# Kernel optimization log

Measured on AMD Instinct MI355X. Metric: run time of the kernel, lower is better.

Reference implementation:

```python
import jax, jax.numpy as jnp
import numpy as np

P = 4       # patch size
NQ = 6      # qubits (2**6 = 64 amplitudes)
NH = 8      # classic attention heads
HD = 8      # head dim (64 / 8)
EPS = 1e-9

_SIGNS = (1.0 - 2.0 * (((np.arange(64)[:, None] >> np.arange(NQ - 1, -1, -1)[None, :]) & 1))).astype(np.float32)  # [64, 6] Z-expectation signs, wire 0 = MSB


def _ln(x, g, b, eps=1e-5):
    m = x.mean(-1, keepdims=True)
    v = x.var(-1, keepdims=True)
    return (x - m) / jnp.sqrt(v + eps) * g + b


def _rot_rx(t):
    c = jnp.cos(t / 2).astype(jnp.complex64)
    s = jnp.sin(t / 2).astype(jnp.complex64)
    return jnp.stack([jnp.stack([c, -1j * s]), jnp.stack([-1j * s, c])])


def _rot_ry(t):
    c = jnp.cos(t / 2).astype(jnp.complex64)
    s = jnp.sin(t / 2).astype(jnp.complex64)
    return jnp.stack([jnp.stack([c, -s]), jnp.stack([s, c])])


def _apply_1q(psi, g, wire):
    # psi: [bsz, 2,2,2,2,2,2]; apply 2x2 unitary g on one wire
    ax = wire + 1
    psi = jnp.moveaxis(psi, ax, -1)
    psi = jnp.einsum('ab,...b->...a', g, psi)
    return jnp.moveaxis(psi, -1, ax)


def _cnot(psi, i):
    # CNOT on adjacent wires [i, i+1]
    cax = i + 1
    p0 = jnp.take(psi, 0, axis=cax)
    p1 = jnp.take(psi, 1, axis=cax)
    p1 = jnp.flip(p1, axis=cax)  # target axis i+2 shifts to cax after removing control axis
    return jnp.stack([p0, p1], axis=cax)


def _pqc(psi, w):
    # RX+RY -> CNOT chain -> RY per layer; w: [depth, NQ, 3]
    for l in range(w.shape[0]):
        for q in range(NQ):
            psi = _apply_1q(psi, _rot_rx(w[l, q, 0]), q)
            psi = _apply_1q(psi, _rot_ry(w[l, q, 1]), q)
        for q in range(NQ - 1):
            psi = _cnot(psi, q)
        for q in range(NQ):
            psi = _apply_1q(psi, _rot_ry(w[l, q, 2]), q)
    return psi


def _probs(psi):
    f = psi.reshape(psi.shape[0], 64)
    return f.real ** 2 + f.imag ** 2


def _measure_z(psi):
    return _probs(psi) @ jnp.asarray(_SIGNS)  # [bsz, 6]


def setup_inputs() -> dict:
    key = jax.random.key(0)
    k = lambda i: jax.random.fold_in(key, i)
    n = lambda i, shp, s=0.02: jax.random.normal(k(i), shp, jnp.float32) * s
    return dict(
        x=jax.random.normal(k(0), (16, 4, 128, 128), jnp.float32),
        conv_w=n(1, (384, 4, P, P)), conv_b=jnp.zeros((384,), jnp.float32),
        ln1_g=jnp.ones(64), ln1_b=jnp.zeros(64),
        wq=n(2, (64, 64)), wk=n(3, (64, 64)), wv=n(4, (64, 64)), wo=n(5, (64, 64)), bo=jnp.zeros(64),
        ln2_g=jnp.ones(64), ln2_b=jnp.zeros(64),
        enc_w=n(6, (2, NQ, 3), 0.1), q_w=n(7, (2, NQ, 3), 0.1), k_w=n(8, (2, NQ, 3), 0.1), v_w=n(9, (2, NQ, 3), 0.1),
        meas_q_w=n(10, (NQ, 3), 0.1), meas_k_w=n(11, (NQ, 3), 0.1), meas_v_w=n(12, (NQ, 3), 0.1),
        qproj_w=n(13, (4, NQ), 0.1), qproj_b=jnp.zeros(4),
        kproj_w=n(14, (4, NQ), 0.1), kproj_b=jnp.zeros(4),
        qkln_g=jnp.ones(4), qkln_b=jnp.zeros(4),
        raw_tau=jnp.asarray(np.log(np.exp(0.5) - 1.0), jnp.float32),
        inp_scale=jnp.ones(64),
        ln3_g=jnp.ones(64), ln3_b=jnp.zeros(64),
        mlp_w1=n(15, (256, 64)), mlp_b1=jnp.zeros(256), mlp_w2=n(16, (64, 256)), mlp_b2=jnp.zeros(64),
    )


def reference(x, conv_w, conv_b, ln1_g, ln1_b, wq, wk, wv, wo, bo, ln2_g, ln2_b,
              enc_w, q_w, k_w, v_w, meas_q_w, meas_k_w, meas_v_w,
              qproj_w, qproj_b, kproj_w, kproj_b, qkln_g, qkln_b, raw_tau, inp_scale,
              ln3_g, ln3_b, mlp_w1, mlp_b1, mlp_w2, mlp_b2):
    B, C, H, W = x.shape
    Hp, Wp = H // P, W // P
    L = Hp * Wp

    # --- PatchEmbed2D: DiT-style conv tokens [B, L, 384] ---
    t384 = jax.lax.conv_general_dilated(x, conv_w, (P, P), 'VALID',
                                        dimension_numbers=('NCHW', 'OIHW', 'NCHW'))
    t384 = t384.reshape(B, -1, L).transpose(0, 2, 1) + conv_b

    # --- PatchEmbed2D: unfold -> amplitude-normalized 64-d tokens ---
    t64 = x.reshape(B, C, Hp, P, Wp, P).transpose(0, 2, 4, 1, 3, 5).reshape(B, L, C * P * P)
    t64 = t64 / (jnp.linalg.norm(t64, axis=-1, keepdims=True) + EPS)

    # --- ClassicAttention64 (manual einsum + softmax MHSA) ---
    hin = _ln(t64, ln1_g, ln1_b)
    q = (hin @ wq.T).reshape(B, L, NH, HD).transpose(0, 2, 1, 3)
    kk = (hin @ wk.T).reshape(B, L, NH, HD).transpose(0, 2, 1, 3)
    v = (hin @ wv.T).reshape(B, L, NH, HD).transpose(0, 2, 1, 3)
    logits = jnp.einsum('bhid,bhjd->bhij', q, kk) * (HD ** -0.5)
    attn = jax.nn.softmax(logits, axis=-1)
    out = jnp.einsum('bhij,bhjd->bhid', attn, v).transpose(0, 2, 1, 3).reshape(B, L, 64)
    h = t64 + (out @ wo.T + bo)

    # --- QuantumAttention64 (QSANN, RBF kernel attention) ---
    xq = _ln(h, ln2_g, ln2_b) * inp_scale
    st = xq.reshape(B * L, 64)
    st = st / (jnp.linalg.norm(st, axis=-1, keepdims=True) + EPS)
    psi0 = st.astype(jnp.complex64).reshape((B * L,) + (2,) * NQ)
    psi_enc = _pqc(psi0, enc_w)
    zq = _measure_z(_pqc(_pqc(psi_enc, q_w), meas_q_w[None]))
    zk = _measure_z(_pqc(_pqc(psi_enc, k_w), meas_k_w[None]))
    pv = _probs(_pqc(_pqc(psi_enc, v_w), meas_v_w[None]))
    v64 = (pv / (pv.sum(-1, keepdims=True) + EPS)).reshape(B, L, 64)
    qv = _ln(zq @ qproj_w.T + qproj_b, qkln_g, qkln_b).reshape(B, L, -1)
    kv = _ln(zk @ kproj_w.T + kproj_b, qkln_g, qkln_b).reshape(B, L, -1)
    tau = jax.nn.softplus(raw_tau)
    d2 = jnp.maximum((qv ** 2).sum(-1)[:, :, None] + (kv ** 2).sum(-1)[:, None, :]
                     - 2.0 * jnp.einsum('bid,bjd->bij', qv, kv), 0.0)
    alpha = jnp.exp(-d2 / tau)
    wts = alpha / (alpha.sum(-1, keepdims=True) + EPS)
    h = h + jnp.einsum('bij,bjd->bid', wts, v64)

    # --- MLP (64 -> 256 -> 64, GELU) ---
    hm = _ln(h, ln3_g, ln3_b)
    h = h + (jax.nn.gelu(hm @ mlp_w1.T + mlp_b1, approximate=True) @ mlp_w2.T + mlp_b2)

    # combine both streams into a single output tensor [B, L, 448]
    return jnp.concatenate([t384, h], axis=-1)
```

## Files before the change

kernel.cpp:

```cpp
#include <hip/hip_runtime.h>

typedef float4 f4;
#define DEV static __device__ __forceinline__

constexpr int Ln = 1024;
constexpr float EPSn = 1e-9f;

typedef __attribute__((ext_vector_type(8))) short short8;
typedef __attribute__((ext_vector_type(16))) float f32x16;
typedef __attribute__((ext_vector_type(4))) unsigned int u32x4;

constexpr size_t OFF_T64 = 0;
constexpr size_t OFF_H   = 1048576;
constexpr size_t OFF_Q   = 2097152;
constexpr size_t OFF_K   = 3145728;
constexpr size_t OFF_V   = 4194304;
constexpr size_t OFF_AO  = 5242880;
constexpr size_t OFF_TR  = 6291456;
constexpr size_t OFF_WQT = OFF_TR + 24576;
constexpr size_t OFF_WKT = OFF_WQT + 4096;
constexpr size_t OFF_WVT = OFF_WKT + 4096;
constexpr size_t OFF_WOT = OFF_WVT + 4096;
constexpr size_t OFF_U   = OFF_WOT + 4096;
constexpr size_t OFF_W2P = OFF_U + 1024;
constexpr size_t OFF_W1P = OFF_W2P + 16384;
constexpr size_t OFF_UT  = OFF_W1P + 16384;

DEV float red16(float v) {
  v += __shfl_xor(v, 1); v += __shfl_xor(v, 2);
  v += __shfl_xor(v, 4); v += __shfl_xor(v, 8);
  return v;
}

DEV unsigned int pk_bf16(float lo, float hi) {
  unsigned int r;
  asm("v_cvt_pk_bf16_f32 %0, %1, %2" : "=v"(r) : "v"(lo), "v"(hi));
  return r;
}

DEV float fast_exp2(float x) {
#if __has_builtin(__builtin_amdgcn_exp2f)
  return __builtin_amdgcn_exp2f(x);
#else
  return __expf(x * 0.6931471805599453f);
#endif
}

__global__ __launch_bounds__(256) void prep_transpose_kernel(
    const float* __restrict__ conv_w, const float* __restrict__ wq,
    const float* __restrict__ wk, const float* __restrict__ wv,
    const float* __restrict__ wo, const float* __restrict__ w1,
    const float* __restrict__ w2, float* __restrict__ ws) {
  int g = blockIdx.x * 256 + threadIdx.x;
  if (g < 24576) {
    int kk = g / 384, o = g % 384;
    ws[OFF_TR + g] = conv_w[o * 64 + kk];
  } else if (g < 40960) {
    int i = g - 24576;
    int m = i >> 12;
    int r = i & 4095;
    int d = r >> 6, o = r & 63;
    const float* src = m == 0 ? wq : m == 1 ? wk : m == 2 ? wv : wo;
    ws[OFF_WQT + i] = src[o * 64 + d];
  } else if (g < 57344) {
    int i = g - 40960;
    int u4 = i >> 8, r = i & 255, o = r >> 2, j = r & 3;
    ws[OFF_W2P + i] = w2[o * 256 + u4 * 4 + j];
  } else if (g < 73728) {
    int i = g - 57344;
    int d4 = i >> 10, r = i & 1023, u = r >> 2, j = r & 3;
    ws[OFF_W1P + i] = w1[u * 64 + d4 * 4 + j];
  }
}

DEV void cmulc(float ar, float ai, float br, float bi, float& cr, float& ci) {
  cr = ar * br - ai * bi; ci = ar * bi + ai * br;
}
DEV void mat2mul(const float* A, const float* B, float* C) {
  for (int i = 0; i < 2; ++i)
    for (int j = 0; j < 2; ++j) {
      float sr = 0.f, si = 0.f;
      for (int kk = 0; kk < 2; ++kk) {
        float pr, pi;
        cmulc(A[(i * 2 + kk) * 2], A[(i * 2 + kk) * 2 + 1],
              B[(kk * 2 + j) * 2], B[(kk * 2 + j) * 2 + 1], pr, pi);
        sr += pr; si += pi;
      }
      C[(i * 2 + j) * 2] = sr; C[(i * 2 + j) * 2 + 1] = si;
    }
}
__global__ void prep_u_kernel(const float* __restrict__ enc_w, const float* __restrict__ q_w,
                              const float* __restrict__ k_w, const float* __restrict__ v_w,
                              const float* __restrict__ mq, const float* __restrict__ mk,
                              const float* __restrict__ mv, float* __restrict__ U) {
  int j = threadIdx.x;
  if (j >= 108) return;
  int branch = j / 36, rem = j % 36, blk = rem / 6, wire = rem % 6;
  const float* bw = branch == 0 ? q_w : branch == 1 ? k_w : v_w;
  const float* mw = branch == 0 ? mq : branch == 1 ? mk : mv;
  auto W = [&](int l, int t) -> float {
    if (l <= 1) return enc_w[(l * 6 + wire) * 3 + t];
    if (l <= 3) return bw[((l - 2) * 6 + wire) * 3 + t];
    return mw[wire * 3 + t];
  };
  auto mk_rx = [](float th, float* M) {
    float c = cosf(0.5f * th), s = sinf(0.5f * th);
    M[0] = c; M[1] = 0; M[2] = 0; M[3] = -s; M[4] = 0; M[5] = -s; M[6] = c; M[7] = 0;
  };
  auto mk_ry = [](float th, float* M) {
    float c = cosf(0.5f * th), s = sinf(0.5f * th);
    M[0] = c; M[1] = 0; M[2] = -s; M[3] = 0; M[4] = s; M[5] = 0; M[6] = c; M[7] = 0;
  };
  float R[8];
  if (blk == 0) {
    float A[8], Bx[8];
    mk_ry(W(0, 1), A); mk_rx(W(0, 0), Bx);
    mat2mul(A, Bx, R);
  } else if (blk <= 4) {
    float A[8], Bx[8], C[8], T[8];
    mk_ry(W(blk, 1), A); mk_rx(W(blk, 0), Bx); mk_ry(W(blk - 1, 2), C);
    mat2mul(Bx, C, T); mat2mul(A, T, R);
  } else {
    mk_ry(W(4, 2), R);
  }
  float* dst = U + ((size_t)(branch * 6 + blk) * 6 + wire) * 8;
  for (int t = 0; t < 8; ++t) dst[t] = R[t];
}

__global__ __launch_bounds__(64) void prep_ubuild_kernel(const float* __restrict__ U,
                                                         float* __restrict__ ut) {
  int branch = blockIdx.x;
  int quad = blockIdx.y;
  int tid = threadIdx.x;
  int s = tid & 3;
  int lane = tid;
  int c = quad * 16 + (tid >> 2);
  bool bit1 = (s & 2) != 0;
  bool bit0 = (s & 1) != 0;
  float re[16], im[16];
#pragma unroll
  for (int i = 0; i < 16; ++i) { re[i] = (s * 16 + i == c) ? 1.f : 0.f; im[i] = 0.f; }
  const float* Ub = U + (size_t)branch * 288;
#pragma unroll 1
  for (int blk = 0; blk < 6; ++blk) {
    const float* Uw = Ub + blk * 48;
    {
      const float* M = Uw;
      float cAr = bit1 ? M[6] : M[0], cAi = bit1 ? M[7] : M[1];
      float cBr = bit1 ? M[4] : M[2], cBi = bit1 ? M[5] : M[3];
#pragma unroll
      for (int i = 0; i < 16; ++i) {
        float pr = __shfl_xor(re[i], 2);
        float pi = __shfl_xor(im[i], 2);
        float nr = cAr * re[i] - cAi * im[i] + cBr * pr - cBi * pi;
        float ni = cAr * im[i] + cAi * re[i] + cBr * pi + cBi * pr;
        re[i] = nr; im[i] = ni;
      }
    }
    {
      const float* M = Uw + 8;
      float cAr = bit0 ? M[6] : M[0], cAi = bit0 ? M[7] : M[1];
      float cBr = bit0 ? M[4] : M[2], cBi = bit0 ? M[5] : M[3];
#pragma unroll
      for (int i = 0; i < 16; ++i) {
        float pr = __shfl_xor(re[i], 1);
        float pi = __shfl_xor(im[i], 1);
        float nr = cAr * re[i] - cAi * im[i] + cBr * pr - cBi * pi;
        float ni = cAr * im[i] + cAi * re[i] + cBr * pi + cBi * pr;
        re[i] = nr; im[i] = ni;
      }
    }
#pragma unroll
    for (int w = 2; w < 6; ++w) {
      const float* M = Uw + w * 8;
      const float m0 = M[0], m1 = M[1], m2 = M[2], m3 = M[3];
      const float m4 = M[4], m5 = M[5], m6 = M[6], m7 = M[7];
      const int mm = 8 >> (w - 2);
#pragma unroll
      for (int i = 0; i < 16; ++i) {
        if (i & mm) continue;
        int i1 = i | mm;
        float ar = re[i], ai = im[i], br = re[i1], bi = im[i1];
        re[i]  = m0 * ar - m1 * ai + m2 * br - m3 * bi;
        im[i]  = m0 * ai + m1 * ar + m2 * bi + m3 * br;
        re[i1] = m4 * ar - m5 * ai + m6 * br - m7 * bi;
        im[i1] = m4 * ai + m5 * ar + m6 * bi + m7 * br;
      }
    }
    if (blk < 5) {
      int sl = (lane & ~3) | (bit1 ? (s ^ 1) : s);
      float tr[16], ti[16];
#pragma unroll
      for (int i = 0; i < 16; ++i) {
        tr[i] = __shfl(re[i], sl);
        ti[i] = __shfl(im[i], sl);
      }
#pragma unroll
      for (int i = 0; i < 16; ++i) {
        int j = i;
        if (j & 2) j ^= 1;
        if (j & 4) j ^= 2;
        if (j & 8) j ^= 4;
        re[i] = bit0 ? tr[j ^ 8] : tr[j];
        im[i] = bit0 ? ti[j ^ 8] : ti[j];
      }
    }
  }
  float* dre = ut + (size_t)branch * 8192 + c * 64 + s * 16;
  float* dim = dre + 4096;
#pragma unroll
  for (int i = 0; i < 16; i += 4) {
    f4 r4 = {re[i], re[i + 1], re[i + 2], re[i + 3]};
    f4 i4 = {im[i], im[i + 1], im[i + 2], im[i + 3]};
    *(f4*)(dre + i) = r4;
    *(f4*)(dim + i) = i4;
  }
}

__global__ __launch_bounds__(256) void patch_kernel(const float* __restrict__ x,
    const float* __restrict__ cwT, const float* __restrict__ conv_b,
    float* __restrict__ out, float* __restrict__ t64) {
  __shared__ float A[64][72];
  __shared__ float scl[64];
  int tid = threadIdx.x;
  int tb = blockIdx.x >> 1;
  int half = blockIdx.x & 1;
  int b = tb >> 4;
  int l0 = (tb & 15) << 6;
  int seg = tid & 15;
  int c = seg >> 2, ph = seg & 3;
#pragma unroll
  for (int r = 0; r < 4; ++r) {
    int tok = (tid >> 4) + (r << 4);
    int l = l0 + tok, hp = l >> 5, wp = l & 31;
    f4 v4 = *(const f4*)(x + (size_t)((b * 4 + c) * 128 + hp * 4 + ph) * 128 + wp * 4);
    A[seg * 4 + 0][tok] = v4.x;
    A[seg * 4 + 1][tok] = v4.y;
    A[seg * 4 + 2][tok] = v4.z;
    A[seg * 4 + 3][tok] = v4.w;
  }
  __syncthreads();
  if (tid < 64) {
    float ss = 0.f;
#pragma unroll
    for (int kk = 0; kk < 64; ++kk) { float vv = A[kk][tid]; ss += vv * vv; }
    scl[tid] = 1.0f / (sqrtf(ss) + EPSn);
  }
  __syncthreads();
  int t0 = tb << 6;
  if (half == 0) {
#pragma unroll
    for (int i = 0; i < 16; ++i) {
      int idx = tid + (i << 8);
      int tok = idx >> 6, kk = idx & 63;
      t64[(size_t)(t0 + tok) * 64 + kk] = A[kk][tok] * scl[tok];
    }
  }
  int tg = tid >> 4;
  int on = (tid & 15) + half * 16;
  float acc[4][12];
#pragma unroll
  for (int i = 0; i < 4; ++i)
#pragma unroll
    for (int jj = 0; jj < 12; ++jj) acc[i][jj] = 0.f;
  for (int kk = 0; kk < 64; ++kk) {
    float a[4];
#pragma unroll
    for (int i = 0; i < 4; ++i) a[i] = A[kk][tg * 4 + i];
    f4 w0 = *(const f4*)(cwT + kk * 384 + on * 12);
    f4 w1 = *(const f4*)(cwT + kk * 384 + on * 12 + 4);
    f4 w2 = *(const f4*)(cwT + kk * 384 + on * 12 + 8);
    float wv_[12] = {w0.x, w0.y, w0.z, w0.w, w1.x, w1.y, w1.z, w1.w, w2.x, w2.y, w2.z, w2.w};
#pragma unroll
    for (int i = 0; i < 4; ++i)
#pragma unroll
      for (int jj = 0; jj < 12; ++jj) acc[i][jj] += a[i] * wv_[jj];
  }
#pragma unroll
  for (int i = 0; i < 4; ++i) {
    int tok = tg * 4 + i;
    size_t basep = (size_t)(t0 + tok) * 448 + on * 12;
#pragma unroll
    for (int jj = 0; jj < 12; ++jj)
      out[basep + jj] = acc[i][jj] + conv_b[on * 12 + jj];
  }
}

__global__ __launch_bounds__(256) void qkv_kernel(const float* __restrict__ t64,
    const float* __restrict__ wqT, const float* __restrict__ wkT, const float* __restrict__ wvT,
    const float* __restrict__ g1, const float* __restrict__ b1,
    float* __restrict__ qo, float* __restrict__ ko, float* __restrict__ vo) {
  __shared__ float wS[12288];
  __shared__ float hin[16][64];
  int tid = threadIdx.x;
#pragma unroll
  for (int p = 0; p < 16; ++p) {
    int idx = p * 256 + tid;
    wS[idx] = wqT[idx];
    wS[4096 + idx] = wkT[idx];
    wS[8192 + idx] = wvT[idx];
  }
  int t0 = blockIdx.x << 4;
  int tt = tid >> 4, part = tid & 15;
  int t = t0 + tt;
  f4 xv = *(const f4*)(t64 + (size_t)t * 64 + part * 4);
  float mean = red16(xv.x + xv.y + xv.z + xv.w) * 0.015625f;
  float d0 = xv.x - mean, d1 = xv.y - mean, d2 = xv.z - mean, d3 = xv.w - mean;
  float var = red16(d0 * d0 + d1 * d1 + d2 * d2 + d3 * d3) * 0.015625f;
  float rs = rsqrtf(var + 1e-5f);
  f4 g4 = *(const f4*)(g1 + part * 4);
  f4 b4 = *(const f4*)(b1 + part * 4);
  f4 hh;
  hh.x = d0 * rs * g4.x + b4.x; hh.y = d1 * rs * g4.y + b4.y;
  hh.z = d2 * rs * g4.z + b4.z; hh.w = d3 * rs * g4.w + b4.w;
  *(f4*)&hin[tt][part * 4] = hh;
  __syncthreads();
  float qa0 = 0, qa1 = 0, qa2 = 0, qa3 = 0;
  float ka0 = 0, ka1 = 0, ka2 = 0, ka3 = 0;
  float va0 = 0, va1 = 0, va2 = 0, va3 = 0;
  for (int d = 0; d < 64; ++d) {
    float hd = hin[tt][d];
    f4 wq4 = *(const f4*)&wS[d * 64 + part * 4];
    f4 wk4 = *(const f4*)&wS[4096 + d * 64 + part * 4];
    f4 wv4 = *(const f4*)&wS[8192 + d * 64 + part * 4];
    qa0 += hd * wq4.x; qa1 += hd * wq4.y; qa2 += hd * wq4.z; qa3 += hd * wq4.w;
    ka0 += hd * wk4.x; ka1 += hd * wk4.y; ka2 += hd * wk4.z; ka3 += hd * wk4.w;
    va0 += hd * wv4.x; va1 += hd * wv4.y; va2 += hd * wv4.z; va3 += hd * wv4.w;
  }
  f4 qr = {qa0, qa1, qa2, qa3}, kr = {ka0, ka1, ka2, ka3}, vr = {va0, va1, va2, va3};
  *(f4*)(qo + (size_t)t * 64 + part * 4) = qr;
  *(f4*)(ko + (size_t)t * 64 + part * 4) = kr;
  *(f4*)(vo + (size_t)t * 64 + part * 4) = vr;
}

__global__ __launch_bounds__(256) void attn_kernel(const float* __restrict__ qg,
    const float* __restrict__ kg, const float* __restrict__ vg, float* __restrict__ ao) {
  __shared__ __align__(16) unsigned short Klds[Ln][8];
  __shared__ __align__(16) unsigned short Vt[10][1032];
  __shared__ __align__(16) unsigned short Qlds[128][8];
  int bh = blockIdx.x;
  int b = bh >> 3, hh = bh & 7;
  int tid = threadIdx.x;
  int qbase = (blockIdx.y << 7);
  const float* kb = kg + (size_t)(b * Ln) * 64 + hh * 8;
  const float* vb = vg + (size_t)(b * Ln) * 64 + hh * 8;
  const float* qb = qg + (size_t)(b * Ln + qbase) * 64 + hh * 8;
  const float SC = 0.51006944f;
#pragma unroll
  for (int p = 0; p < 8; ++p) {
    int e4 = p * 256 + tid;
    int j = e4 >> 1, part = e4 & 1;
    f4 kv = *(const f4*)(kb + (size_t)j * 64 + part * 4);
    *(uint2*)&Klds[j][part * 4] =
        make_uint2(pk_bf16(kv.x * SC, kv.y * SC), pk_bf16(kv.z * SC, kv.w * SC));
    f4 vv = *(const f4*)(vb + (size_t)j * 64 + part * 4);
    unsigned int u01 = pk_bf16(vv.x, vv.y), u23 = pk_bf16(vv.z, vv.w);
    int d0 = part * 4;
    Vt[d0 + 0][j] = (unsigned short)u01;
    Vt[d0 + 1][j] = (unsigned short)(u01 >> 16);
    Vt[d0 + 2][j] = (unsigned short)u23;
    Vt[d0 + 3][j] = (unsigned short)(u23 >> 16);
  }
#pragma unroll
  for (int p = 0; p < 4; ++p) {
    int j = p * 256 + tid;
    Vt[8][j] = 0x3F80;
    Vt[9][j] = 0;
  }
  {
    int j = tid >> 1, part = tid & 1;
    f4 qv = *(const f4*)(qb + (size_t)j * 64 + part * 4);
    *(uint2*)&Qlds[j][part * 4] = make_uint2(pk_bf16(qv.x, qv.y), pk_bf16(qv.z, qv.w));
  }
  __syncthreads();

  int l = tid & 63, w = tid >> 6;
  int lq = l & 31;
  bool lo = l < 32;
  const short8 zero8 = {0, 0, 0, 0, 0, 0, 0, 0};
  short8 qf = *(const short8*)&Qlds[w * 32 + lq][0];
  qf = lo ? qf : zero8;
  int d = lq;
  int dc = d > 9 ? 9 : d;
  int vrow0 = (l >> 5) * 8;
  f32x16 acc = {};
  const f32x16 fz = {};
  for (int t = 0; t < 32; ++t) {
    short8 kf = *(const short8*)&Klds[t * 32 + lq][0];
    kf = lo ? kf : zero8;
    f32x16 s = __builtin_amdgcn_mfma_f32_32x32x16_bf16(kf, qf, fz, 0, 0, 0);
    float p[16];
#pragma unroll
    for (int r = 0; r < 16; ++r) p[r] = fast_exp2(s[r]);
    unsigned int c0 = pk_bf16(p[0], p[1]),  c1 = pk_bf16(p[2], p[3]);
    unsigned int c2 = pk_bf16(p[4], p[5]),  c3 = pk_bf16(p[6], p[7]);
    unsigned int c4 = pk_bf16(p[8], p[9]),  c5 = pk_bf16(p[10], p[11]);
    unsigned int c6 = pk_bf16(p[12], p[13]), c7 = pk_bf16(p[14], p[15]);
    unsigned int x0 = c0, y0 = c2;
    asm("v_permlane32_swap_b32 %0, %1" : "+v"(x0), "+v"(y0));
    unsigned int x1 = c1, y1 = c3;
    asm("v_permlane32_swap_b32 %0, %1" : "+v"(x1), "+v"(y1));
    unsigned int x4 = c4, y4 = c6;
    asm("v_permlane32_swap_b32 %0, %1" : "+v"(x4), "+v"(y4));
    unsigned int x5 = c5, y5 = c7;
    asm("v_permlane32_swap_b32 %0, %1" : "+v"(x5), "+v"(y5));
    union { u32x4 u; short8 s8; } B0, B1;
    B0.u = (u32x4){x0, x1, y0, y1};
    B1.u = (u32x4){x4, x5, y4, y5};
    int jb = t * 32 + vrow0;
    short8 av0 = *(const short8*)&Vt[dc][jb];
    short8 av1 = *(const short8*)&Vt[dc][jb + 16];
    acc = __builtin_amdgcn_mfma_f32_32x32x16_bf16(av0, B0.s8, acc, 0, 0, 0);
    acc = __builtin_amdgcn_mfma_f32_32x32x16_bf16(av1, B1.s8, acc, 0, 0, 0);
  }
  float ssum = __shfl(acc[4], lq);
  float inv = 1.0f / ssum;
  f4 o = {acc[0] * inv, acc[1] * inv, acc[2] * inv, acc[3] * inv};
  float* dst = ao + (size_t)(b * Ln + qbase + w * 32 + lq) * 64 + hh * 8 + (lo ? 0 : 4);
  *(f4*)dst = o;
}

__global__ __launch_bounds__(256) void proj_st_kernel(float* __restrict__ t64st,
    const float* __restrict__ ao, const float* __restrict__ woT, const float* __restrict__ bo,
    const float* __restrict__ g2, const float* __restrict__ b2, const float* __restrict__ iscale,
    float* __restrict__ hB) {
  __shared__ float woS[4096];
  __shared__ float aos[16][64];
  int tid = threadIdx.x;
#pragma unroll
  for (int p = 0; p < 16; ++p) {
    int idx = p * 256 + tid;
    woS[idx] = woT[idx];
  }
  int t0 = blockIdx.x << 4;
  int tt = tid >> 4, part = tid & 15;
  int t = t0 + tt;
  *(f4*)&aos[tt][part * 4] = *(const f4*)(ao + (size_t)t * 64 + part * 4);
  __syncthreads();
  f4 acc;
  acc.x = bo[part * 4 + 0]; acc.y = bo[part * 4 + 1];
  acc.z = bo[part * 4 + 2]; acc.w = bo[part * 4 + 3];
  for (int d = 0; d < 64; ++d) {
    float ad = aos[tt][d];
    f4 w4 = *(const f4*)&woS[d * 64 + part * 4];
    acc.x += ad * w4.x; acc.y += ad * w4.y; acc.z += ad * w4.z; acc.w += ad * w4.w;
  }
  f4 tv = *(const f4*)(t64st + (size_t)t * 64 + part * 4);
  f4 hv = {tv.x + acc.x, tv.y + acc.y, tv.z + acc.z, tv.w + acc.w};
  *(f4*)(hB + (size_t)t * 64 + part * 4) = hv;
  float mean = red16(hv.x + hv.y + hv.z + hv.w) * 0.015625f;
  float d0 = hv.x - mean, d1 = hv.y - mean, d2 = hv.z - mean, d3 = hv.w - mean;
  float var = red16(d0 * d0 + d1 * d1 + d2 * d2 + d3 * d3) * 0.015625f;
  float rs = rsqrtf(var + 1e-5f);
  f4 g4 = *(const f4*)(g2 + part * 4);
  f4 b4 = *(const f4*)(b2 + part * 4);
  f4 is4 = *(const f4*)(iscale + part * 4);
  float x0 = (d0 * rs * g4.x + b4.x) * is4.x;
  float x1 = (d1 * rs * g4.y + b4.y) * is4.y;
  float x2 = (d2 * rs * g4.z + b4.z) * is4.z;
  float x3 = (d3 * rs * g4.w + b4.w) * is4.w;
  float nrm = sqrtf(red16(x0 * x0 + x1 * x1 + x2 * x2 + x3 * x3));
  float rn = 1.0f / (nrm + EPSn);
  f4 stv = {x0 * rn, x1 * rn, x2 * rn, x3 * rn};
  *(f4*)(t64st + (size_t)t * 64 + part * 4) = stv;
}

__global__ __launch_bounds__(256) void quantum_kernel(const float* __restrict__ st,
    const float* __restrict__ ut,
    const float* __restrict__ qproj_w, const float* __restrict__ qproj_b,
    const float* __restrict__ kproj_w, const float* __restrict__ kproj_b,
    const float* __restrict__ qkg, const float* __restrict__ qkb,
    float* __restrict__ qvb, float* __restrict__ kvb, float* __restrict__ v64) {
  __shared__ float smem[12288];
  int tid = threadIdx.x;
  int branch = blockIdx.y;
  int t0 = blockIdx.x << 6;
  const float* ub = ut + (size_t)branch * 8192;
#pragma unroll
  for (int p = 0; p < 16; ++p) {
    int idx = p * 256 + tid;
    smem[idx] = st[(size_t)t0 * 64 + idx];
    smem[4096 + idx] = ub[idx];
    smem[8192 + idx] = ub[4096 + idx];
  }
  __syncthreads();
  int o = tid & 63, tg = tid >> 6;
  float accre[16], accim[16];
#pragma unroll
  for (int i = 0; i < 16; ++i) { accre[i] = 0.f; accim[i] = 0.f; }
  for (int k4 = 0; k4 < 16; ++k4) {
    float ur[4], ui[4];
#pragma unroll
    for (int j = 0; j < 4; ++j) {
      ur[j] = smem[4096 + (k4 * 4 + j) * 64 + o];
      ui[j] = smem[8192 + (k4 * 4 + j) * 64 + o];
    }
#pragma unroll
    for (int tt = 0; tt < 16; ++tt) {
      f4 a = *(const f4*)&smem[(tg * 16 + tt) * 64 + k4 * 4];
      accre[tt] += a.x * ur[0] + a.y * ur[1] + a.z * ur[2] + a.w * ur[3];
      accim[tt] += a.x * ui[0] + a.y * ui[1] + a.z * ui[2] + a.w * ui[3];
    }
  }
  __syncthreads();
#pragma unroll
  for (int tt = 0; tt < 16; ++tt) {
    int t = tg * 16 + tt;
    smem[t * 65 + o] = accre[tt] * accre[tt] + accim[tt] * accim[tt];
  }
  __syncthreads();
  int s = tid & 3;
  int tokL = tid >> 2;
  int token = t0 + tokL;
  bool bit1 = (s & 2) != 0;
  bool bit0 = (s & 1) != 0;
  float p[16];
#pragma unroll
  for (int i = 0; i < 16; ++i) p[i] = smem[tokL * 65 + s * 16 + i];
  float lsum = 0.f;
#pragma unroll
  for (int i = 0; i < 16; ++i) lsum += p[i];
  if (branch == 2) {
    float tot = lsum;
    tot += __shfl_xor(tot, 1);
    tot += __shfl_xor(tot, 2);
    float rn = 1.0f / (tot + EPSn);
    float* dst = v64 + (size_t)token * 64 + s * 16;
#pragma unroll
    for (int i = 0; i < 16; i += 4) {
      f4 o4 = {p[i] * rn, p[i + 1] * rn, p[i + 2] * rn, p[i + 3] * rn};
      *(f4*)(dst + i) = o4;
    }
  } else {
    float lz[4] = {0.f, 0.f, 0.f, 0.f};
#pragma unroll
    for (int i = 0; i < 16; ++i) {
      lz[0] += (i & 8) ? -p[i] : p[i];
      lz[1] += (i & 4) ? -p[i] : p[i];
      lz[2] += (i & 2) ? -p[i] : p[i];
      lz[3] += (i & 1) ? -p[i] : p[i];
    }
    float z[6];
    float u0 = bit1 ? -lsum : lsum;
    u0 += __shfl_xor(u0, 1); u0 += __shfl_xor(u0, 2); z[0] = u0;
    float u1 = bit0 ? -lsum : lsum;
    u1 += __shfl_xor(u1, 1); u1 += __shfl_xor(u1, 2); z[1] = u1;
#pragma unroll
    for (int q = 0; q < 4; ++q) {
      float v = lz[q];
      v += __shfl_xor(v, 1); v += __shfl_xor(v, 2);
      z[2 + q] = v;
    }
    const float* pw = branch == 0 ? qproj_w : kproj_w;
    const float* pb = branch == 0 ? qproj_b : kproj_b;
    float pr4[4];
#pragma unroll
    for (int jj = 0; jj < 4; ++jj) {
      float a = pb[jj];
#pragma unroll
      for (int qq = 0; qq < 6; ++qq) a += z[qq] * pw[jj * 6 + qq];
      pr4[jj] = a;
    }
    float mean = (pr4[0] + pr4[1] + pr4[2] + pr4[3]) * 0.25f;
    float var = 0.f;
#pragma unroll
    for (int jj = 0; jj < 4; ++jj) { float dd = pr4[jj] - mean; var += dd * dd; }
    var *= 0.25f;
    float rs = rsqrtf(var + 1e-5f);
    if (s == 0) {
      f4 o4;
      o4.x = (pr4[0] - mean) * rs * qkg[0] + qkb[0];
      o4.y = (pr4[1] - mean) * rs * qkg[1] + qkb[1];
      o4.z = (pr4[2] - mean) * rs * qkg[2] + qkb[2];
      o4.w = (pr4[3] - mean) * rs * qkg[3] + qkb[3];
      *(f4*)((branch == 0 ? qvb : kvb) + (size_t)token * 4) = o4;
    }
  }
}

__global__ __launch_bounds__(256) void rbf_kernel(const float* __restrict__ qvb,
    const float* __restrict__ kvb, const float* __restrict__ v64,
    const float* __restrict__ raw_tau, float* __restrict__ pacc, float* __restrict__ pasum) {
  __shared__ __align__(16) unsigned short Vlds[512][64];
  __shared__ __align__(16) unsigned short kvbs[512][8];
  __shared__ float kks[512];
  int tid = threadIdx.x;
  int q0 = blockIdx.x << 7;
  int b = q0 >> 10;
  int kc = blockIdx.y;
  float tau = log1pf(__expf(raw_tau[0]));
  float inv_tau = 1.0f / tau;
  float inv2t = 2.0f * inv_tau;
  int kbase = b * Ln + (kc << 9);
#pragma unroll
  for (int p = 0; p < 2; ++p) {
    int j = p * 256 + tid;
    f4 kv4 = *(const f4*)(kvb + (size_t)(kbase + j) * 4);
    kks[j] = (kv4.x * kv4.x + kv4.y * kv4.y + kv4.z * kv4.z + kv4.w * kv4.w) * inv_tau;
    *(uint4*)&kvbs[j][0] = make_uint4(pk_bf16(kv4.x, kv4.y), pk_bf16(kv4.z, kv4.w), 0u, 0u);
  }
#pragma unroll
  for (int it = 0; it < 32; ++it) {
    int idx = it * 256 + tid;
    int row = idx >> 4, c4 = idx & 15;
    f4 vv = *(const f4*)(v64 + (size_t)(kbase + row) * 64 + c4 * 4);
    *(uint2*)&Vlds[row][c4 * 4] = make_uint2(pk_bf16(vv.x, vv.y), pk_bf16(vv.z, vv.w));
  }
  __syncthreads();

  int l = tid & 63, w = tid >> 6;
  int lq = l & 31;
  bool lo = l < 32;
  bool hi = !lo;
  const short8 zero8 = {0, 0, 0, 0, 0, 0, 0, 0};
  int qtok = q0 + w * 32 + lq;
  f4 qv4 = *(const f4*)(qvb + (size_t)qtok * 4);
  union { u32x4 u; short8 s8; } Qf;
  Qf.u = (u32x4){pk_bf16(qv4.x, qv4.y), pk_bf16(qv4.z, qv4.w), 0u, 0u};
  short8 qf = lo ? Qf.s8 : zero8;
  int vrow0 = (l >> 5) * 8;
  int dbase = hi ? 4 : 0;
  f32x16 acc0 = {}, acc1 = {};
  const f32x16 fz = {};
  float dsum = 0.f;
  for (int t = 0; t < 16; ++t) {
    short8 kf = lo ? *(const short8*)&kvbs[t * 32 + lq][0] : zero8;
    f32x16 s = __builtin_amdgcn_mfma_f32_32x32x16_bf16(kf, qf, fz, 0, 0, 0);
    int rowbase = t * 32 + dbase;
    float p[16];
#pragma unroll
    for (int r = 0; r < 16; ++r) {
      float kkv = kks[rowbase + (r & 3) + 8 * (r >> 2)];
      p[r] = __expf(s[r] * inv2t - kkv);
      dsum += p[r];
    }
    unsigned int c0 = pk_bf16(p[0], p[1]),  c1 = pk_bf16(p[2], p[3]);
    unsigned int c2 = pk_bf16(p[4], p[5]),  c3 = pk_bf16(p[6], p[7]);
    unsigned int c4 = pk_bf16(p[8], p[9]),  c5 = pk_bf16(p[10], p[11]);
    unsigned int c6 = pk_bf16(p[12], p[13]), c7 = pk_bf16(p[14], p[15]);
    unsigned int pc0 = (unsigned int)__shfl((int)c0, l ^ 32);
    unsigned int pc1 = (unsigned int)__shfl((int)c1, l ^ 32);
    unsigned int pc2 = (unsigned int)__shfl((int)c2, l ^ 32);
    unsigned int pc3 = (unsigned int)__shfl((int)c3, l ^ 32);
    unsigned int pc4 = (unsigned int)__shfl((int)c4, l ^ 32);
    unsigned int pc5 = (unsigned int)__shfl((int)c5, l ^ 32);
    unsigned int pc6 = (unsigned int)__shfl((int)c6, l ^ 32);
    unsigned int pc7 = (unsigned int)__shfl((int)c7, l ^ 32);
    union { u32x4 u; short8 s8; } B0, B1;
    B0.u = lo ? (u32x4){c0, c1, pc0, pc1} : (u32x4){pc2, pc3, c2, c3};
    B1.u = lo ? (u32x4){c4, c5, pc4, pc5} : (u32x4){pc6, pc7, c6, c7};
    int jb = t * 32 + vrow0;
    short8 a00, a10, a01, a11;
#pragma unroll
    for (int e = 0; e < 8; ++e) {
      a00[e] = (short)Vlds[jb + e][lq];
      a10[e] = (short)Vlds[jb + e][32 + lq];
      a01[e] = (short)Vlds[jb + 16 + e][lq];
      a11[e] = (short)Vlds[jb + 16 + e][32 + lq];
    }
    acc0 = __builtin_amdgcn_mfma_f32_32x32x16_bf16(a00, B0.s8, acc0, 0, 0, 0);
    acc1 = __builtin_amdgcn_mfma_f32_32x32x16_bf16(a10, B0.s8, acc1, 0, 0, 0);
    acc0 = __builtin_amdgcn_mfma_f32_32x32x16_bf16(a01, B1.s8, acc0, 0, 0, 0);
    acc1 = __builtin_amdgcn_mfma_f32_32x32x16_bf16(a11, B1.s8, acc1, 0, 0, 0);
  }
  float dtot = dsum + __shfl_xor(dsum, 32);
  if (lo) pasum[(kc << 14) + qtok] = dtot;
  float* pa = pacc + (size_t)kc * 1048576 + (size_t)qtok * 64;
#pragma unroll
  for (int r = 0; r < 16; ++r) {
    int dd = (r & 3) + 8 * (r >> 2) + dbase;
    pa[dd] = acc0[r];
    pa[32 + dd] = acc1[r];
  }
}

__global__ __launch_bounds__(256) void m0m1_kernel(float* __restrict__ hB,
    const float* __restrict__ pacc, const float* __restrict__ pasum,
    const float* __restrict__ g3, const float* __restrict__ b3,
    const float* __restrict__ w1p, const float* __restrict__ b1v,
    float* __restrict__ hid) {
  __shared__ float hmS[16][64];
  int tid = threadIdx.x;
  int t0 = blockIdx.x << 4;
  {
    int tt = tid >> 4, part = tid & 15;
    int t = t0 + tt;
    f4 hv = *(const f4*)(hB + (size_t)t * 64 + part * 4);
    f4 p0 = *(const f4*)(pacc + (size_t)t * 64 + part * 4);
    f4 p1 = *(const f4*)(pacc + 1048576 + (size_t)t * 64 + part * 4);
    float rden = 1.0f / (pasum[t] + pasum[16384 + t] + EPSn);
    hv.x += (p0.x + p1.x) * rden; hv.y += (p0.y + p1.y) * rden;
    hv.z += (p0.z + p1.z) * rden; hv.w += (p0.w + p1.w) * rden;
    *(f4*)(hB + (size_t)t * 64 + part * 4) = hv;
    float mean = red16(hv.x + hv.y + hv.z + hv.w) * 0.015625f;
    float d0 = hv.x - mean, d1 = hv.y - mean, d2 = hv.z - mean, d3 = hv.w - mean;
    float var = red16(d0 * d0 + d1 * d1 + d2 * d2 + d3 * d3) * 0.015625f;
    float rs = rsqrtf(var + 1e-5f);
    f4 g4 = *(const f4*)(g3 + part * 4);
    f4 b4 = *(const f4*)(b3 + part * 4);
    f4 o4 = {d0 * rs * g4.x + b4.x, d1 * rs * g4.y + b4.y,
             d2 * rs * g4.z + b4.z, d3 * rs * g4.w + b4.w};
    *(f4*)&hmS[tt][part * 4] = o4;
  }
  __syncthreads();
  int u = tid;
  float wrow[64];
#pragma unroll
  for (int d4 = 0; d4 < 16; ++d4) {
    f4 w4 = *(const f4*)(w1p + d4 * 1024 + u * 4);
    wrow[d4 * 4] = w4.x; wrow[d4 * 4 + 1] = w4.y;
    wrow[d4 * 4 + 2] = w4.z; wrow[d4 * 4 + 3] = w4.w;
  }
  float bias = b1v[u];
  for (int tok = 0; tok < 16; ++tok) {
    const float* hr = hmS[tok];
    float a0 = 0.f, a1 = 0.f, a2 = 0.f, a3 = 0.f;
#pragma unroll
    for (int d = 0; d < 64; d += 4) {
      a0 += hr[d] * wrow[d];
      a1 += hr[d + 1] * wrow[d + 1];
      a2 += hr[d + 2] * wrow[d + 2];
      a3 += hr[d + 3] * wrow[d + 3];
    }
    float a = bias + ((a0 + a1) + (a2 + a3));
    float tz = 0.7978845608028654f * (a + 0.044715f * a * a * a);
    float e = __expf(2.0f * tz);
    float th = 1.0f - 2.0f / (e + 1.0f);
    hid[(size_t)(t0 + tok) * 256 + u] = 0.5f * a * (1.0f + th);
  }
}

__global__ __launch_bounds__(256) void m2_kernel(const float* __restrict__ hB,
    const float* __restrict__ hid, const float* __restrict__ w2p, const float* __restrict__ b2v,
    float* __restrict__ out) {
  __shared__ float hidS[32][256];
  int tid = threadIdx.x;
  int t0 = blockIdx.x << 5;
#pragma unroll
  for (int p = 0; p < 8; ++p) {
    int idx = p * 256 + tid;
    int tok = idx >> 6, u4 = idx & 63;
    *(f4*)&hidS[tok][u4 * 4] = *(const f4*)(hid + (size_t)(t0 + tok) * 256 + u4 * 4);
  }
  __syncthreads();
  int o = tid & 63, tg = tid >> 6;
  f4 acc[8];
#pragma unroll
  for (int tt = 0; tt < 8; ++tt) acc[tt] = {0.f, 0.f, 0.f, 0.f};
#pragma unroll 4
  for (int u4 = 0; u4 < 64; ++u4) {
    f4 wv = *(const f4*)(w2p + u4 * 256 + o * 4);
#pragma unroll
    for (int tt = 0; tt < 8; ++tt) {
      f4 hv = *(const f4*)&hidS[tg * 8 + tt][u4 * 4];
      acc[tt].x += hv.x * wv.x; acc[tt].y += hv.y * wv.y;
      acc[tt].z += hv.z * wv.z; acc[tt].w += hv.w * wv.w;
    }
  }
  float bb = b2v[o];
#pragma unroll
  for (int tt = 0; tt < 8; ++tt) {
    int t = t0 + tg * 8 + tt;
    float r = bb + ((acc[tt].x + acc[tt].y) + (acc[tt].z + acc[tt].w));
    out[(size_t)t * 448 + 384 + o] = hB[(size_t)t * 64 + o] + r;
  }
}

extern "C" void kernel_launch(void* const* d_in, const int* in_sizes, int n_in,
                              void* d_out, int out_size, void* d_ws, size_t ws_size,
                              hipStream_t stream) {
  (void)in_sizes; (void)n_in; (void)out_size; (void)ws_size;
  const float* x       = (const float*)d_in[0];
  const float* conv_w  = (const float*)d_in[1];
  const float* conv_b  = (const float*)d_in[2];
  const float* ln1_g   = (const float*)d_in[3];
  const float* ln1_b   = (const float*)d_in[4];
  const float* wq      = (const float*)d_in[5];
  const float* wk      = (const float*)d_in[6];
  const float* wv      = (const float*)d_in[7];
  const float* wo      = (const float*)d_in[8];
  const float* bo      = (const float*)d_in[9];
  const float* ln2_g   = (const float*)d_in[10];
  const float* ln2_b   = (const float*)d_in[11];
  const float* enc_w   = (const float*)d_in[12];
  const float* q_w     = (const float*)d_in[13];
  const float* k_w     = (const float*)d_in[14];
  const float* v_w     = (const float*)d_in[15];
  const float* mq_w    = (const float*)d_in[16];
  const float* mk_w    = (const float*)d_in[17];
  const float* mv_w    = (const float*)d_in[18];
  const float* qproj_w = (const float*)d_in[19];
  const float* qproj_b = (const float*)d_in[20];
  const float* kproj_w = (const float*)d_in[21];
  const float* kproj_b = (const float*)d_in[22];
  const float* qkln_g  = (const float*)d_in[23];
  const float* qkln_b  = (const float*)d_in[24];
  const float* raw_tau = (const float*)d_in[25];
  const float* iscale  = (const float*)d_in[26];
  const float* ln3_g   = (const float*)d_in[27];
  const float* ln3_b   = (const float*)d_in[28];
  const float* mlp_w1  = (const float*)d_in[29];
  const float* mlp_b1  = (const float*)d_in[30];
  const float* mlp_w2  = (const float*)d_in[31];
  const float* mlp_b2  = (const float*)d_in[32];
  float* out = (float*)d_out;
  float* ws  = (float*)d_ws;

  prep_transpose_kernel<<<288, 256, 0, stream>>>(conv_w, wq, wk, wv, wo, mlp_w1, mlp_w2, ws);
  prep_u_kernel<<<1, 128, 0, stream>>>(enc_w, q_w, k_w, v_w, mq_w, mk_w, mv_w, ws + OFF_U);
  prep_ubuild_kernel<<<dim3(3, 4), 64, 0, stream>>>(ws + OFF_U, ws + OFF_UT);
  patch_kernel<<<512, 256, 0, stream>>>(x, ws + OFF_TR, conv_b, out, ws + OFF_T64);
  qkv_kernel<<<1024, 256, 0, stream>>>(ws + OFF_T64, ws + OFF_WQT, ws + OFF_WKT, ws + OFF_WVT,
                                       ln1_g, ln1_b, ws + OFF_Q, ws + OFF_K, ws + OFF_V);
  attn_kernel<<<dim3(128, 8), 256, 0, stream>>>(ws + OFF_Q, ws + OFF_K, ws + OFF_V, ws + OFF_AO);
  proj_st_kernel<<<1024, 256, 0, stream>>>(ws + OFF_T64, ws + OFF_AO, ws + OFF_WOT, bo,
                                           ln2_g, ln2_b, iscale, ws + OFF_H);
  quantum_kernel<<<dim3(256, 3), 256, 0, stream>>>(ws + OFF_T64, ws + OFF_UT,
                                                   qproj_w, qproj_b, kproj_w, kproj_b,
                                                   qkln_g, qkln_b,
                                                   ws + OFF_K, ws + OFF_K + 65536, ws + OFF_Q);
  rbf_kernel<<<dim3(128, 2), 256, 0, stream>>>(ws + OFF_K, ws + OFF_K + 65536, ws + OFF_Q,
                                               raw_tau, ws + OFF_V, ws + OFF_K + 131072);
  m0m1_kernel<<<1024, 256, 0, stream>>>(ws + OFF_H, ws + OFF_V, ws + OFF_K + 131072,
                                        ln3_g, ln3_b, ws + OFF_W1P, mlp_b1, ws + OFF_Q);
  m2_kernel<<<512, 256, 0, stream>>>(ws + OFF_H, ws + OFF_Q, ws + OFF_W2P, mlp_b2, out);
}
```

Before: 195.7 us.

## Merge prep kernels into one launch and streamline RBF attention inner loop

Three small weight-preparation launches become one kernel: the gate matrices are built in shared memory and consumed in the same block, which removes two launches and a global round trip. In the RBF kernel, V is stored transposed in LDS so MFMA operands load as single 16-byte vectors instead of eight scalar reads. The 2/tau and log2(e) scaling is folded into the bf16 K operand so the exponential becomes a bare exp2. The eight cross-half shuffles are replaced with four v_permlane32_swap instructions. The transposed LDS fill uses scattered 2-byte stores that may bank-conflict, and folding the scale before bf16 rounding slightly changes numerics.

```diff
diff --git a/kernel.cpp b/kernel.cpp
--- a/kernel.cpp
+++ b/kernel.cpp
@@ -46,33 +46,6 @@
 #endif
 }
 
-__global__ __launch_bounds__(256) void prep_transpose_kernel(
-    const float* __restrict__ conv_w, const float* __restrict__ wq,
-    const float* __restrict__ wk, const float* __restrict__ wv,
-    const float* __restrict__ wo, const float* __restrict__ w1,
-    const float* __restrict__ w2, float* __restrict__ ws) {
-  int g = blockIdx.x * 256 + threadIdx.x;
-  if (g < 24576) {
-    int kk = g / 384, o = g % 384;
-    ws[OFF_TR + g] = conv_w[o * 64 + kk];
-  } else if (g < 40960) {
-    int i = g - 24576;
-    int m = i >> 12;
-    int r = i & 4095;
-    int d = r >> 6, o = r & 63;
-    const float* src = m == 0 ? wq : m == 1 ? wk : m == 2 ? wv : wo;
-    ws[OFF_WQT + i] = src[o * 64 + d];
-  } else if (g < 57344) {
-    int i = g - 40960;
-    int u4 = i >> 8, r = i & 255, o = r >> 2, j = r & 3;
-    ws[OFF_W2P + i] = w2[o * 256 + u4 * 4 + j];
-  } else if (g < 73728) {
-    int i = g - 57344;
-    int d4 = i >> 10, r = i & 1023, u = r >> 2, j = r & 3;
-    ws[OFF_W1P + i] = w1[u * 64 + d4 * 4 + j];
-  }
-}
-
 DEV void cmulc(float ar, float ai, float br, float bi, float& cr, float& ci) {
   cr = ar * br - ai * bi; ci = ar * bi + ai * br;
 }
@@ -89,49 +62,78 @@
       C[(i * 2 + j) * 2] = sr; C[(i * 2 + j) * 2 + 1] = si;
     }
 }
-__global__ void prep_u_kernel(const float* __restrict__ enc_w, const float* __restrict__ q_w,
-                              const float* __restrict__ k_w, const float* __restrict__ v_w,
-                              const float* __restrict__ mq, const float* __restrict__ mk,
-                              const float* __restrict__ mv, float* __restrict__ U) {
-  int j = threadIdx.x;
-  if (j >= 108) return;
-  int branch = j / 36, rem = j % 36, blk = rem / 6, wire = rem % 6;
+
+__global__ __launch_bounds__(256) void prep_all_kernel(
+    const float* __restrict__ conv_w, const float* __restrict__ wq,
+    const float* __restrict__ wk, const float* __restrict__ wv,
+    const float* __restrict__ wo, const float* __restrict__ w1,
+    const float* __restrict__ w2,
+    const float* __restrict__ enc_w, const float* __restrict__ q_w,
+    const float* __restrict__ k_w, const float* __restrict__ v_w,
+    const float* __restrict__ mq, const float* __restrict__ mk,
+    const float* __restrict__ mv, float* __restrict__ ws) {
+  __shared__ float Ulds[288];
+  int bx = blockIdx.x;
+  int tid = threadIdx.x;
+  if (bx < 288) {
+    int g = bx * 256 + tid;
+    if (g < 24576) {
+      int kk = g / 384, o = g % 384;
+      ws[OFF_TR + g] = conv_w[o * 64 + kk];
+    } else if (g < 40960) {
+      int i = g - 24576;
+      int m = i >> 12;
+      int r = i & 4095;
+      int d = r >> 6, o = r & 63;
+      const float* src = m == 0 ? wq : m == 1 ? wk : m == 2 ? wv : wo;
+      ws[OFF_WQT + i] = src[o * 64 + d];
+    } else if (g < 57344) {
+      int i = g - 40960;
+      int u4 = i >> 8, r = i & 255, o = r >> 2, j = r & 3;
+      ws[OFF_W2P + i] = w2[o * 256 + u4 * 4 + j];
+    } else if (g < 73728) {
+      int i = g - 57344;
+      int d4 = i >> 10, r = i & 1023, u = r >> 2, j = r & 3;
+      ws[OFF_W1P + i] = w1[u * 64 + d4 * 4 + j];
+    }
+    return;
+  }
+  int ub = bx - 288;
+  int branch = ub >> 2, quad = ub & 3;
   const float* bw = branch == 0 ? q_w : branch == 1 ? k_w : v_w;
   const float* mw = branch == 0 ? mq : branch == 1 ? mk : mv;
-  auto W = [&](int l, int t) -> float {
-    if (l <= 1) return enc_w[(l * 6 + wire) * 3 + t];
-    if (l <= 3) return bw[((l - 2) * 6 + wire) * 3 + t];
-    return mw[wire * 3 + t];
-  };
-  auto mk_rx = [](float th, float* M) {
-    float c = cosf(0.5f * th), s = sinf(0.5f * th);
-    M[0] = c; M[1] = 0; M[2] = 0; M[3] = -s; M[4] = 0; M[5] = -s; M[6] = c; M[7] = 0;
-  };
-  auto mk_ry = [](float th, float* M) {
-    float c = cosf(0.5f * th), s = sinf(0.5f * th);
-    M[0] = c; M[1] = 0; M[2] = -s; M[3] = 0; M[4] = s; M[5] = 0; M[6] = c; M[7] = 0;
-  };
-  float R[8];
-  if (blk == 0) {
-    float A[8], Bx[8];
-    mk_ry(W(0, 1), A); mk_rx(W(0, 0), Bx);
-    mat2mul(A, Bx, R);
-  } else if (blk <= 4) {
-    float A[8], Bx[8], C[8], T[8];
-    mk_ry(W(blk, 1), A); mk_rx(W(blk, 0), Bx); mk_ry(W(blk - 1, 2), C);
-    mat2mul(Bx, C, T); mat2mul(A, T, R);
-  } else {
-    mk_ry(W(4, 2), R);
-  }
-  float* dst = U + ((size_t)(branch * 6 + blk) * 6 + wire) * 8;
-  for (int t = 0; t < 8; ++t) dst[t] = R[t];
-}
-
-__global__ __launch_bounds__(64) void prep_ubuild_kernel(const float* __restrict__ U,
-                                                         float* __restrict__ ut) {
-  int branch = blockIdx.x;
-  int quad = blockIdx.y;
-  int tid = threadIdx.x;
+  if (tid < 36) {
+    int blk = tid / 6, wire = tid % 6;
+    auto W = [&](int l, int t) -> float {
+      if (l <= 1) return enc_w[(l * 6 + wire) * 3 + t];
+      if (l <= 3) return bw[((l - 2) * 6 + wire) * 3 + t];
+      return mw[wire * 3 + t];
+    };
+    auto mk_rx = [](float th, float* M) {
+      float c = cosf(0.5f * th), s = sinf(0.5f * th);
+      M[0] = c; M[1] = 0; M[2] = 0; M[3] = -s; M[4] = 0; M[5] = -s; M[6] = c; M[7] = 0;
+    };
+    auto mk_ry = [](float th, float* M) {
+      float c = cosf(0.5f * th), s = sinf(0.5f * th);
+      M[0] = c; M[1] = 0; M[2] = -s; M[3] = 0; M[4] = s; M[5] = 0; M[6] = c; M[7] = 0;
+    };
+    float R[8];
+    if (blk == 0) {
+      float A[8], Bx[8];
+      mk_ry(W(0, 1), A); mk_rx(W(0, 0), Bx);
+      mat2mul(A, Bx, R);
+    } else if (blk <= 4) {
+      float A[8], Bx[8], C[8], T[8];
+      mk_ry(W(blk, 1), A); mk_rx(W(blk, 0), Bx); mk_ry(W(blk - 1, 2), C);
+      mat2mul(Bx, C, T); mat2mul(A, T, R);
+    } else {
+      mk_ry(W(4, 2), R);
+    }
+#pragma unroll
+    for (int t = 0; t < 8; ++t) Ulds[(blk * 6 + wire) * 8 + t] = R[t];
+  }
+  __syncthreads();
+  if (tid >= 64) return;
   int s = tid & 3;
   int lane = tid;
   int c = quad * 16 + (tid >> 2);
@@ -140,10 +142,9 @@
   float re[16], im[16];
 #pragma unroll
   for (int i = 0; i < 16; ++i) { re[i] = (s * 16 + i == c) ? 1.f : 0.f; im[i] = 0.f; }
-  const float* Ub = U + (size_t)branch * 288;
 #pragma unroll 1
   for (int blk = 0; blk < 6; ++blk) {
-    const float* Uw = Ub + blk * 48;
+    const float* Uw = Ulds + blk * 48;
     {
       const float* M = Uw;
       float cAr = bit1 ? M[6] : M[0], cAi = bit1 ? M[7] : M[1];
@@ -206,7 +207,7 @@
       }
     }
   }
-  float* dre = ut + (size_t)branch * 8192 + c * 64 + s * 16;
+  float* dre = ws + OFF_UT + (size_t)branch * 8192 + c * 64 + s * 16;
   float* dim = dre + 4096;
 #pragma unroll
   for (int i = 0; i < 16; i += 4) {
@@ -581,7 +582,7 @@
 __global__ __launch_bounds__(256) void rbf_kernel(const float* __restrict__ qvb,
     const float* __restrict__ kvb, const float* __restrict__ v64,
     const float* __restrict__ raw_tau, float* __restrict__ pacc, float* __restrict__ pasum) {
-  __shared__ __align__(16) unsigned short Vlds[512][64];
+  __shared__ __align__(16) unsigned short Vt[64][520];
   __shared__ __align__(16) unsigned short kvbs[512][8];
   __shared__ float kks[512];
   int tid = threadIdx.x;
@@ -589,22 +590,28 @@
   int b = q0 >> 10;
   int kc = blockIdx.y;
   float tau = log1pf(__expf(raw_tau[0]));
-  float inv_tau = 1.0f / tau;
-  float inv2t = 2.0f * inv_tau;
+  const float L2E = 1.4426950408889634f;
+  float sck = 2.0f * L2E / tau;
   int kbase = b * Ln + (kc << 9);
 #pragma unroll
   for (int p = 0; p < 2; ++p) {
     int j = p * 256 + tid;
     f4 kv4 = *(const f4*)(kvb + (size_t)(kbase + j) * 4);
-    kks[j] = (kv4.x * kv4.x + kv4.y * kv4.y + kv4.z * kv4.z + kv4.w * kv4.w) * inv_tau;
-    *(uint4*)&kvbs[j][0] = make_uint4(pk_bf16(kv4.x, kv4.y), pk_bf16(kv4.z, kv4.w), 0u, 0u);
+    kks[j] = (kv4.x * kv4.x + kv4.y * kv4.y + kv4.z * kv4.z + kv4.w * kv4.w) * (L2E / tau);
+    *(uint4*)&kvbs[j][0] =
+        make_uint4(pk_bf16(kv4.x * sck, kv4.y * sck), pk_bf16(kv4.z * sck, kv4.w * sck), 0u, 0u);
   }
 #pragma unroll
   for (int it = 0; it < 32; ++it) {
     int idx = it * 256 + tid;
     int row = idx >> 4, c4 = idx & 15;
     f4 vv = *(const f4*)(v64 + (size_t)(kbase + row) * 64 + c4 * 4);
-    *(uint2*)&Vlds[row][c4 * 4] = make_uint2(pk_bf16(vv.x, vv.y), pk_bf16(vv.z, vv.w));
+    unsigned int u01 = pk_bf16(vv.x, vv.y), u23 = pk_bf16(vv.z, vv.w);
+    int d0 = c4 * 4;
+    Vt[d0 + 0][row] = (unsigned short)u01;
+    Vt[d0 + 1][row] = (unsigned short)(u01 >> 16);
+    Vt[d0 + 2][row] = (unsigned short)u23;
+    Vt[d0 + 3][row] = (unsigned short)(u23 >> 16);
   }
   __syncthreads();
 
@@ -631,33 +638,29 @@
 #pragma unroll
     for (int r = 0; r < 16; ++r) {
       float kkv = kks[rowbase + (r & 3) + 8 * (r >> 2)];
-      p[r] = __expf(s[r] * inv2t - kkv);
+      p[r] = fast_exp2(s[r] - kkv);
       dsum += p[r];
     }
     unsigned int c0 = pk_bf16(p[0], p[1]),  c1 = pk_bf16(p[2], p[3]);
     unsigned int c2 = pk_bf16(p[4], p[5]),  c3 = pk_bf16(p[6], p[7]);
     unsigned int c4 = pk_bf16(p[8], p[9]),  c5 = pk_bf16(p[10], p[11]);
     unsigned int c6 = pk_bf16(p[12], p[13]), c7 = pk_bf16(p[14], p[15]);
-    unsigned int pc0 = (unsigned int)__shfl((int)c0, l ^ 32);
-    unsigned int pc1 = (unsigned int)__shfl((int)c1, l ^ 32);
-    unsigned int pc2 = (unsigned int)__shfl((int)c2, l ^ 32);
-    unsigned int pc3 = (unsigned int)__shfl((int)c3, l ^ 32);
-    unsigned int pc4 = (unsigned int)__shfl((int)c4, l ^ 32);
-    unsigned int pc5 = (unsigned int)__shfl((int)c5, l ^ 32);
-    unsigned int pc6 = (unsigned int)__shfl((int)c6, l ^ 32);
-    unsigned int pc7 = (unsigned int)__shfl((int)c7, l ^ 32);
+    unsigned int x0 = c0, y0 = c2;
+    asm("v_permlane32_swap_b32 %0, %1" : "+v"(x0), "+v"(y0));
+    unsigned int x1 = c1, y1 = c3;
+    asm("v_permlane32_swap_b32 %0, %1" : "+v"(x1), "+v"(y1));
+    unsigned int x4 = c4, y4 = c6;
+    asm("v_permlane32_swap_b32 %0, %1" : "+v"(x4), "+v"(y4));
+    unsigned int x5 = c5, y5 = c7;
+    asm("v_permlane32_swap_b32 %0, %1" : "+v"(x5), "+v"(y5));
     union { u32x4 u; short8 s8; } B0, B1;
-    B0.u = lo ? (u32x4){c0, c1, pc0, pc1} : (u32x4){pc2, pc3, c2, c3};
-    B1.u = lo ? (u32x4){c4, c5, pc4, pc5} : (u32x4){pc6, pc7, c6, c7};
+    B0.u = (u32x4){x0, x1, y0, y1};
+    B1.u = (u32x4){x4, x5, y4, y5};
     int jb = t * 32 + vrow0;
-    short8 a00, a10, a01, a11;
-#pragma unroll
-    for (int e = 0; e < 8; ++e) {
-      a00[e] = (short)Vlds[jb + e][lq];
-      a10[e] = (short)Vlds[jb + e][32 + lq];
-      a01[e] = (short)Vlds[jb + 16 + e][lq];
-      a11[e] = (short)Vlds[jb + 16 + e][32 + lq];
-    }
+    short8 a00 = *(const short8*)&Vt[lq][jb];
+    short8 a10 = *(const short8*)&Vt[32 + lq][jb];
+    short8 a01 = *(const short8*)&Vt[lq][jb + 16];
+    short8 a11 = *(const short8*)&Vt[32 + lq][jb + 16];
     acc0 = __builtin_amdgcn_mfma_f32_32x32x16_bf16(a00, B0.s8, acc0, 0, 0, 0);
     acc1 = __builtin_amdgcn_mfma_f32_32x32x16_bf16(a10, B0.s8, acc1, 0, 0, 0);
     acc0 = __builtin_amdgcn_mfma_f32_32x32x16_bf16(a01, B1.s8, acc0, 0, 0, 0);
@@ -806,9 +809,8 @@
   float* out = (float*)d_out;
   float* ws  = (float*)d_ws;
 
-  prep_transpose_kernel<<<288, 256, 0, stream>>>(conv_w, wq, wk, wv, wo, mlp_w1, mlp_w2, ws);
-  prep_u_kernel<<<1, 128, 0, stream>>>(enc_w, q_w, k_w, v_w, mq_w, mk_w, mv_w, ws + OFF_U);
-  prep_ubuild_kernel<<<dim3(3, 4), 64, 0, stream>>>(ws + OFF_U, ws + OFF_UT);
+  prep_all_kernel<<<300, 256, 0, stream>>>(conv_w, wq, wk, wv, wo, mlp_w1, mlp_w2,
+                                           enc_w, q_w, k_w, v_w, mq_w, mk_w, mv_w, ws);
   patch_kernel<<<512, 256, 0, stream>>>(x, ws + OFF_TR, conv_b, out, ws + OFF_T64);
   qkv_kernel<<<1024, 256, 0, stream>>>(ws + OFF_T64, ws + OFF_WQT, ws + OFF_WKT, ws + OFF_WVT,
                                        ln1_g, ln1_b, ws + OFF_Q, ws + OFF_K, ws + OFF_V);
```

New measurement: 186.4 us. -4.8%, faster.
